# Optimization experiments

Hardware: AMD Instinct MI355X
Metric: run time of the kernel (lower is better)

Reference implementation:

```python
import jax, jax.numpy as jnp
import numpy as np

B, H_IMG, W_IMG = 8, 64, 64
C, HEADS, SR, MSG = 128, 4, 4, 4
N0 = H_IMG * W_IMG


def _linear(x, w, b):
    return x @ w.T + b


def _layernorm(x, g, b, eps=1e-5):
    mu = jnp.mean(x, -1, keepdims=True)
    var = jnp.mean(jnp.square(x - mu), -1, keepdims=True)
    return (x - mu) * jax.lax.rsqrt(var + eps) * g + b


def _conv2d(x, w, b, stride, pad, groups=1):
    y = jax.lax.conv_general_dilated(
        x, w, (stride, stride), [(pad, pad), (pad, pad)],
        dimension_numbers=("NCHW", "OIHW", "NCHW"), feature_group_count=groups)
    return y + b[None, :, None, None]


def setup_inputs():
    key = jax.random.key(0)
    ks = jax.random.split(key, 16)
    def nrm(k, shape, std=0.02):
        return jax.random.normal(k, shape, jnp.float32) * std
    z = lambda *s: jnp.zeros(s, jnp.float32)
    return {
        "x": jax.random.normal(ks[0], (B, N0, C), jnp.float32),
        "msg_tokens": jax.random.normal(ks[1], (B, MSG, C), jnp.float32),
        "Wq": nrm(ks[2], (C, C)), "bq": z(C),
        "sr1_w": nrm(ks[3], (C, C, 4, 4), float(np.sqrt(2.0 / (16 * C)))), "sr1_b": z(C),
        "ln1_g": jnp.ones((C,), jnp.float32), "ln1_b": z(C),
        "sr2_w": nrm(ks[4], (C, C, 2, 2), float(np.sqrt(2.0 / (4 * C)))), "sr2_b": z(C),
        "ln2_g": jnp.ones((C,), jnp.float32), "ln2_b": z(C),
        "kv1_w": nrm(ks[5], (C, C)), "kv1_b": z(C),
        "kv2_w": nrm(ks[6], (C, C)), "kv2_b": z(C),
        "lc1_w": nrm(ks[7], (C // 2, 1, 3, 3), float(np.sqrt(2.0 / 9.0))), "lc1_b": z(C // 2),
        "lc2_w": nrm(ks[8], (C // 2, 1, 3, 3), float(np.sqrt(2.0 / 9.0))), "lc2_b": z(C // 2),
        "proj_w": nrm(ks[9], (C, C)), "proj_b": z(C),
        "H": H_IMG, "W": W_IMG,
    }


def reference(x, msg_tokens, Wq, bq, sr1_w, sr1_b, ln1_g, ln1_b,
              sr2_w, sr2_b, ln2_g, ln2_b, kv1_w, kv1_b, kv2_w, kv2_b,
              lc1_w, lc1_b, lc2_w, lc2_b, proj_w, proj_b, H, W):
    Bsz, _, Cc = x.shape
    m = msg_tokens.shape[1]
    h = HEADS
    dh = Cc // h
    scale = dh ** -0.5
    x_q = jnp.concatenate([x, msg_tokens], axis=1)       # [B, N, C]
    N = x_q.shape[1]
    q = _linear(x_q, Wq, bq).reshape(Bsz, N, h, dh).transpose(0, 2, 1, 3)  # [B,h,N,dh]
    x_img = x.transpose(0, 2, 1).reshape(Bsz, Cc, H, W)

    def branch(sr_w, sr_b, ln_g, ln_b, kv_w, kv_b, lc_w, lc_b, q_half, stride):
        Hr, Wr = H // stride, W // stride
        L = Hr * Wr
        # spatial reduction conv -> tokens
        xr = _conv2d(x_img, sr_w, sr_b, stride, 0).reshape(Bsz, Cc, L).transpose(0, 2, 1)
        # message tokens pass through the SR conv via summed weights
        msg_r = jnp.einsum('bnc,oc->bno', msg_tokens, sr_w.sum((-1, -2))) + sr_b
        xk = jax.nn.gelu(_layernorm(jnp.concatenate([xr, msg_r], 1), ln_g, ln_b), approximate=False)
        kv = _linear(xk, kv_w, kv_b).reshape(Bsz, L + m, 2, h // 2, dh).transpose(2, 0, 3, 1, 4)
        k, v = kv[0], kv[1]                               # [B, h/2, L+m, dh]
        attn = jax.nn.softmax(jnp.einsum('bhnd,bhld->bhnl', q_half, k) * scale, axis=-1)
        # fused depthwise conv on the spatial part of V (message tokens bypass)
        v_flat = v.transpose(0, 2, 1, 3).reshape(Bsz, L + m, Cc // 2).transpose(0, 2, 1)  # [B,C/2,L+m]
        lc = _conv2d(v_flat[:, :, :L].reshape(Bsz, Cc // 2, Hr, Wr), lc_w, lc_b, 1, 1,
                     groups=Cc // 2).reshape(Bsz, Cc // 2, L)
        v_add = jnp.concatenate([lc, v_flat[:, :, L:]], axis=2)
        v = v + v_add.reshape(Bsz, h // 2, dh, L + m).transpose(0, 1, 3, 2)
        return jnp.einsum('bhnl,bhld->bhnd', attn, v).transpose(0, 2, 1, 3).reshape(Bsz, N, Cc // 2)

    x1 = branch(sr1_w, sr1_b, ln1_g, ln1_b, kv1_w, kv1_b, lc1_w, lc1_b, q[:, :h // 2], SR)
    x2 = branch(sr2_w, sr2_b, ln2_g, ln2_b, kv2_w, kv2_b, lc2_w, lc2_b, q[:, h // 2:], SR // 2)
    out = _linear(jnp.concatenate([x1, x2], -1), proj_w, proj_b)
    out = x_q + out                                       # identity = x_q, drop_path = Identity
    return out[:, :-m], out[:, -m:]
```

## Files before the change

### kernel.cpp

```cpp
#include <hip/hip_runtime.h>
#include <math.h>

#define BB 8
#define CC 128
#define N0 4096
#define MSGN 4
#define NTOT 4100
#define IMG 64
#define NPAD 4224
#define LMP1 320
#define LMP2 1088

#define OFF_WFQ    0
#define OFF_WFKV1  8192
#define OFF_WFKV2  16384
#define OFF_WFPROJ 24576
#define OFF_WFSR1  32768
#define OFF_WFSR2  163840
#define OFF_QH     196608
#define OFF_XK1    2359296
#define OFF_XK2    2492416
#define OFF_KV1O   3018752
#define OFF_KV2O   3284992
#define OFF_KH1    4337664
#define OFF_VT1    4419584
#define OFF_KH2    4501504
#define OFF_VT2    4780032
#define OFF_XP     5058560

typedef _Float16 half8v __attribute__((ext_vector_type(8)));
typedef _Float16 half4v __attribute__((ext_vector_type(4)));
typedef float f32x4 __attribute__((ext_vector_type(4)));

__device__ __forceinline__ size_t af_idx(int m, int k, int Kc) {
    return ((size_t)((m >> 4) * Kc + (k >> 5)) * 64 + ((k >> 3) & 3) * 16 + (m & 15)) * 8 + (k & 7);
}

__device__ __forceinline__ float exp2_fast(float x) {
#if __has_builtin(__builtin_amdgcn_exp2f)
    return __builtin_amdgcn_exp2f(x);
#else
    return __expf(x * 0.6931471805599453f);
#endif
}

__device__ __forceinline__ void gload16(const _Float16* g, _Float16* l) {
    __builtin_amdgcn_global_load_lds(
        (const __attribute__((address_space(1))) unsigned int*)g,
        (__attribute__((address_space(3))) unsigned int*)l, 16, 0, 0);
}

__global__ void prep_weights(const float* __restrict__ Wq, const float* __restrict__ kv1,
                             const float* __restrict__ kv2, const float* __restrict__ proj,
                             const float* __restrict__ sr1w, const float* __restrict__ sr2w,
                             float* __restrict__ ws, _Float16* __restrict__ Qh,
                             _Float16* __restrict__ Kh1, _Float16* __restrict__ Kh2) {
    int u = blockIdx.x * blockDim.x + threadIdx.x;
    if (u >= 176128) {
        int e = u - 176128;
        int d = e & 31;
        int rest = e >> 5;
        if (rest < 960) {
            int n = 260 + rest % 60;
            int bh = rest / 60;
            Kh1[((size_t)bh * LMP1 + n) * 32 + d] = (_Float16)0.f;
        } else {
            rest -= 960;
            int n = 1028 + rest % 60;
            int bh = rest / 60;
            Kh2[((size_t)bh * LMP2 + n) * 32 + d] = (_Float16)0.f;
        }
        return;
    }
    if (u >= 49152) {
        int idx = u - 49152;
        int d = idx & 31;
        int rest = idx >> 5;
        int n = NTOT + rest % (NPAD - NTOT);
        int rest2 = rest / (NPAD - NTOT);
        int hg = rest2 & 3;
        int b = rest2 >> 2;
        Qh[((size_t)(b * 4 + hg) * NPAD + n) * 32 + d] = (_Float16)0.f;
        return;
    }
    int seg, base;
    const float* w = nullptr;
    _Float16* dst;
    if (u < 2048)        { seg = 0; base = u;          w = Wq;   dst = (_Float16*)(ws + OFF_WFQ); }
    else if (u < 4096)   { seg = 0; base = u - 2048;   w = kv1;  dst = (_Float16*)(ws + OFF_WFKV1); }
    else if (u < 6144)   { seg = 0; base = u - 4096;   w = kv2;  dst = (_Float16*)(ws + OFF_WFKV2); }
    else if (u < 8192)   { seg = 0; base = u - 6144;   w = proj; dst = (_Float16*)(ws + OFF_WFPROJ); }
    else if (u < 40960)  { seg = 1; base = u - 8192;   w = sr1w; dst = (_Float16*)(ws + OFF_WFSR1); }
    else                 { seg = 2; base = u - 40960;  w = sr2w; dst = (_Float16*)(ws + OFF_WFSR2); }
    int lane = base & 63;
    int t = (base >> 6) & 7;
    int kc = base >> 9;
    int n = t * 16 + (lane & 15);
    int k0 = kc * 32 + (lane >> 4) * 8;
    half8v val;
    #pragma unroll
    for (int j = 0; j < 8; ++j) {
        int k = k0 + j;
        float v;
        if (seg == 0) v = w[n * 128 + k];
        else if (seg == 1) v = w[(n * 128 + (k & 127)) * 16 + (k >> 7)];
        else v = w[(n * 128 + (k & 127)) * 4 + (k >> 7)];
        val[j] = (_Float16)v;
    }
    *(half8v*)(dst + (size_t)base * 8) = val;
}

template<int S, int WR, int LL, int LM, int KW>
__device__ __forceinline__ void sr_partial(
    int mtile, int kcbase, int lane, const float* __restrict__ x,
    const float* __restrict__ msg, const _Float16* __restrict__ Wf, f32x4 acc[8]) {
    int m15 = lane & 15, quadk = lane >> 4;
    int m = mtile * 16 + m15;
    bool valid = m < BB * LM;
    const float* base = x;
    bool isimg = false;
    if (valid) {
        int b = m / LM, tok = m - b * LM;
        if (tok < LL) {
            int hr = tok / WR, wr = tok - hr * WR;
            base = x + ((size_t)b * N0 + hr * S * IMG + wr * S) * 128;
            isimg = true;
        } else {
            base = msg + ((size_t)b * MSGN + (tok - LL)) * 128;
        }
    }
    const half8v* Bp = (const half8v*)Wf + lane;
    for (int kk = 0; kk < KW; ++kk) {
        int kc = kcbase + kk;
        int k0 = (kc * 4 + quadk) * 8;
        int c = k0 & 127, ij = k0 >> 7;
        half8v a;
        if (valid) {
            int off;
            if (isimg) {
                int ki = ij / S, kj = ij - ki * S;
                off = (ki * IMG + kj) * 128 + c;
            } else off = c;
            const float4* p4 = (const float4*)(base + off);
            float4 f0 = p4[0], f1 = p4[1];
            a[0] = (_Float16)f0.x; a[1] = (_Float16)f0.y; a[2] = (_Float16)f0.z; a[3] = (_Float16)f0.w;
            a[4] = (_Float16)f1.x; a[5] = (_Float16)f1.y; a[6] = (_Float16)f1.z; a[7] = (_Float16)f1.w;
        } else {
            #pragma unroll
            for (int j = 0; j < 8; ++j) a[j] = (_Float16)0.f;
        }
        #pragma unroll
        for (int t = 0; t < 8; ++t)
            acc[t] = __builtin_amdgcn_mfma_f32_16x16x32_f16(a, Bp[(size_t)(kc * 8 + t) * 64], acc[t], 0, 0, 0);
    }
}

__global__ __launch_bounds__(256) void input_gemms(
    const float* __restrict__ x, const float* __restrict__ msg,
    const _Float16* __restrict__ Wf1, const _Float16* __restrict__ Wf2,
    const float* __restrict__ b1, const float* __restrict__ g1, const float* __restrict__ be1,
    const float* __restrict__ b2, const float* __restrict__ g2, const float* __restrict__ be2,
    const _Float16* __restrict__ WfKV1, const _Float16* __restrict__ WfKV2,
    const float* __restrict__ kvb1, const float* __restrict__ kvb2,
    _Float16* __restrict__ Kh1, float* __restrict__ vo1,
    _Float16* __restrict__ Kh2, float* __restrict__ vo2,
    const _Float16* __restrict__ WfQ, const float* __restrict__ bq,
    _Float16* __restrict__ Qh) {
    __shared__ float red[4][2048];
    int tid = threadIdx.x;
    int lane = tid & 63, wave = tid >> 6;
    int bid = blockIdx.x;
    const f32x4 zf4 = {0.f, 0.f, 0.f, 0.f};

    if (bid >= 261) {
        int u = (bid - 261) * 4 + wave;
        int mt = u >> 1, nh = u & 1;
        int m15 = lane & 15, quadk = lane >> 4;
        int m = mt * 16 + m15;
        bool valid = m < BB * NTOT;
        const float* rowp = x;
        if (valid) {
            int b = m / NTOT, n = m - b * NTOT;
            rowp = (n < N0) ? (x + ((size_t)b * N0 + n) * 128)
                            : (msg + ((size_t)b * MSGN + (n - N0)) * 128);
        }
        const half8v* Bp = (const half8v*)WfQ + lane;
        f32x4 acc[4];
        #pragma unroll
        for (int t = 0; t < 4; ++t) acc[t] = zf4;
        #pragma unroll
        for (int kc = 0; kc < 4; ++kc) {
            half8v a;
            if (valid) {
                const float4* p4 = (const float4*)(rowp + (kc * 4 + quadk) * 8);
                float4 f0 = p4[0], f1 = p4[1];
                a[0] = (_Float16)f0.x; a[1] = (_Float16)f0.y; a[2] = (_Float16)f0.z; a[3] = (_Float16)f0.w;
                a[4] = (_Float16)f1.x; a[5] = (_Float16)f1.y; a[6] = (_Float16)f1.z; a[7] = (_Float16)f1.w;
            } else {
                #pragma unroll
                for (int j = 0; j < 8; ++j) a[j] = (_Float16)0.f;
            }
            #pragma unroll
            for (int t = 0; t < 4; ++t)
                acc[t] = __builtin_amdgcn_mfma_f32_16x16x32_f16(a, Bp[(size_t)(kc * 8 + nh * 4 + t) * 64], acc[t], 0, 0, 0);
        }
        int quad = lane >> 4, n15 = lane & 15;
        const float qscale = 0.17677669529663687f * 1.4426950408889634f;
        #pragma unroll
        for (int r = 0; r < 4; ++r) {
            int mm = mt * 16 + quad * 4 + r;
            if (mm >= BB * NTOT) continue;
            int b = mm / NTOT, tok = mm - b * NTOT;
            #pragma unroll
            for (int t = 0; t < 4; ++t) {
                int n = nh * 64 + t * 16 + n15;
                Qh[((size_t)(b * 4 + (n >> 5)) * NPAD + tok) * 32 + (n & 31)] =
                    (_Float16)((acc[t][r] + bq[n]) * qscale);
            }
        }
        return;
    }

    if (bid >= 132) {
        int mtile = (bid - 132) * 4 + wave;
        f32x4 acc[8];
        #pragma unroll
        for (int t = 0; t < 8; ++t) acc[t] = zf4;
        sr_partial<2, 32, 1024, 1028, 16>(mtile, 0, lane, x, msg, Wf2, acc);
        int quad = lane >> 4, n15 = lane & 15;
        float bb[8], gg[8], eb[8];
        #pragma unroll
        for (int j = 0; j < 8; ++j) {
            bb[j] = b2[j * 16 + n15];
            gg[j] = g2[j * 16 + n15];
            eb[j] = be2[j * 16 + n15];
        }
        _Float16* XKw = (_Float16*)(&red[0][0]) + wave * 2176;
        #pragma unroll
        for (int r = 0; r < 4; ++r) {
            float s = 0.f;
            #pragma unroll
            for (int j = 0; j < 8; ++j) s += acc[j][r] + bb[j];
            #pragma unroll
            for (int off = 1; off < 16; off <<= 1) s += __shfl_xor(s, off);
            float mu = s * (1.f / 128.f);
            float q = 0.f;
            #pragma unroll
            for (int j = 0; j < 8; ++j) { float d = acc[j][r] + bb[j] - mu; q += d * d; }
            #pragma unroll
            for (int off = 1; off < 16; off <<= 1) q += __shfl_xor(q, off);
            float rs = rsqrtf(q * (1.f / 128.f) + 1e-5f);
            #pragma unroll
            for (int j = 0; j < 8; ++j) {
                float y = (acc[j][r] + bb[j] - mu) * rs * gg[j] + eb[j];
                y = 0.5f * y * (1.f + erff(y * 0.70710678118654752f));
                XKw[(quad * 4 + r) * 136 + j * 16 + n15] = (_Float16)y;
            }
        }
        __syncthreads();
        const half8v* Bp = (const half8v*)WfKV2 + lane;
        f32x4 ka[8];
        #pragma unroll
        for (int tt = 0; tt < 8; ++tt) ka[tt] = zf4;
        #pragma unroll
        for (int kc = 0; kc < 4; ++kc) {
            half8v a = *(const half8v*)&XKw[(lane & 15) * 136 + kc * 32 + (lane >> 4) * 8];
            #pragma unroll
            for (int tt = 0; tt < 8; ++tt)
                ka[tt] = __builtin_amdgcn_mfma_f32_16x16x32_f16(a, Bp[(size_t)(kc * 8 + tt) * 64], ka[tt], 0, 0, 0);
        }
        #pragma unroll
        for (int r = 0; r < 4; ++r) {
            int m = mtile * 16 + quad * 4 + r;
            if (m >= 8224) continue;
            int b = m / 1028, tok = m - b * 1028;
            #pragma unroll
            for (int tt = 0; tt < 8; ++tt) {
                int n = tt * 16 + n15;
                float val = ka[tt][r] + kvb2[n];
                if (tt < 4) {
                    Kh2[((size_t)(b * 2 + (n >> 5)) * LMP2 + tok) * 32 + (n & 31)] = (_Float16)val;
                } else {
                    vo2[((size_t)b * 1028 + tok) * 64 + (n - 64)] = val;
                }
            }
        }
        return;
    }

    f32x4 acc[8];
    #pragma unroll
    for (int t = 0; t < 8; ++t) acc[t] = zf4;
    int mtile = bid;
    sr_partial<4, 16, 256, 260, 16>(mtile, wave * 16, lane, x, msg, Wf1, acc);
    int quad = lane >> 4, n15 = lane & 15;
    #pragma unroll
    for (int t = 0; t < 8; ++t)
        #pragma unroll
        for (int r = 0; r < 4; ++r)
            red[wave][(quad * 4 + r) * 128 + t * 16 + n15] = acc[t][r];
    __syncthreads();
    for (int e = tid; e < 2048; e += 256)
        red[0][e] = red[0][e] + red[1][e] + red[2][e] + red[3][e];
    __syncthreads();
    int r16 = tid >> 4, l16 = tid & 15;
    int m = mtile * 16 + r16;
    float v[8];
    float s = 0.f;
    #pragma unroll
    for (int j = 0; j < 8; ++j) { v[j] = red[0][r16 * 128 + j * 16 + l16] + b1[j * 16 + l16]; s += v[j]; }
    #pragma unroll
    for (int off = 1; off < 16; off <<= 1) s += __shfl_xor(s, off);
    float mu = s * (1.f / 128.f);
    float q = 0.f;
    #pragma unroll
    for (int j = 0; j < 8; ++j) { v[j] -= mu; q += v[j] * v[j]; }
    #pragma unroll
    for (int off = 1; off < 16; off <<= 1) q += __shfl_xor(q, off);
    float rs = rsqrtf(q * (1.f / 128.f) + 1e-5f);
    _Float16* XKs = (_Float16*)(&red[1][0]);
    if (m < 2080) {
        #pragma unroll
        for (int j = 0; j < 8; ++j) {
            float y = v[j] * rs * g1[j * 16 + l16] + be1[j * 16 + l16];
            y = 0.5f * y * (1.f + erff(y * 0.70710678118654752f));
            XKs[r16 * 136 + j * 16 + l16] = (_Float16)y;
        }
    }
    __syncthreads();
    {
        const half8v* Bp = (const half8v*)WfKV1 + lane;
        int t0 = wave * 2;
        f32x4 ka[2];
        ka[0] = zf4; ka[1] = zf4;
        #pragma unroll
        for (int kc = 0; kc < 4; ++kc) {
            half8v a = *(const half8v*)&XKs[(lane & 15) * 136 + kc * 32 + (lane >> 4) * 8];
            #pragma unroll
            for (int tt = 0; tt < 2; ++tt)
                ka[tt] = __builtin_amdgcn_mfma_f32_16x16x32_f16(a, Bp[(size_t)(kc * 8 + t0 + tt) * 64], ka[tt], 0, 0, 0);
        }
        #pragma unroll
        for (int r = 0; r < 4; ++r) {
            int mm = mtile * 16 + quad * 4 + r;
            if (mm >= 2080) continue;
            int b = mm / 260, tok = mm - b * 260;
            #pragma unroll
            for (int tt = 0; tt < 2; ++tt) {
                int n = (t0 + tt) * 16 + n15;
                float val = ka[tt][r] + kvb1[n];
                if (n < 64) {
                    Kh1[((size_t)(b * 2 + (n >> 5)) * LMP1 + tok) * 32 + (n & 31)] = (_Float16)val;
                } else {
                    vo1[((size_t)b * 260 + tok) * 64 + (n - 64)] = val;
                }
            }
        }
    }
}

__global__ void pack_kv(const float* __restrict__ vo1, const float* __restrict__ vo2,
                        const float* __restrict__ lc1w, const float* __restrict__ lc1b,
                        const float* __restrict__ lc2w, const float* __restrict__ lc2b,
                        _Float16* __restrict__ Vt1, _Float16* __restrict__ Vt2) {
    int idx = blockIdx.x * 256 + threadIdx.x;
    const int T1 = BB * LMP1 * 64;
    const float* vo;
    const float* lcw;
    const float* lcb;
    _Float16* Vt;
    int Wr, L, Lm, Lmp, li;
    if (idx < T1) { li = idx;      vo = vo1; lcw = lc1w; lcb = lc1b; Vt = Vt1; Wr = 16; L = 256;  Lm = 260;  Lmp = LMP1; }
    else          { li = idx - T1; vo = vo2; lcw = lc2w; lcb = lc2b; Vt = Vt2; Wr = 32; L = 1024; Lm = 1028; Lmp = LMP2; }
    int ch = li & 63;
    int rest = li >> 6;
    int n = rest % Lmp;
    int b = rest / Lmp;
    int h2 = ch >> 5, d = ch & 31;
    int Hr = L / Wr;
    float vnew = 0.f;
    if (n < Lm) {
        const float* vb2 = vo + (size_t)b * Lm * 64;
        float v = vb2[(size_t)n * 64 + ch];
        float add;
        if (n < L) {
            int hr = n / Wr, wr = n - hr * Wr;
            float sum = lcb[ch];
            #pragma unroll
            for (int ki = 0; ki < 3; ++ki)
                #pragma unroll
                for (int kj = 0; kj < 3; ++kj) {
                    int y = hr + ki - 1, xx = wr + kj - 1;
                    if ((unsigned)y < (unsigned)Hr && (unsigned)xx < (unsigned)Wr)
                        sum += lcw[ch * 9 + ki * 3 + kj] * vb2[((size_t)y * Wr + xx) * 64 + ch];
                }
            add = sum;
        } else {
            add = v;
        }
        vnew = v + add;
    }
    Vt[(size_t)(b * 2 + h2) * Lmp * 32 + (size_t)(n >> 2) * 128
       + (d & 15) * 8 + ((d >> 4) << 2) + (n & 3)] = (_Float16)vnew;
}

__global__ __launch_bounds__(256, 4) void attn_mfma(
    const _Float16* __restrict__ Qh,
    const _Float16* __restrict__ Kh1, const _Float16* __restrict__ Vt1,
    const _Float16* __restrict__ Kh2, const _Float16* __restrict__ Vt2,
    _Float16* __restrict__ XP) {
    __shared__ _Float16 sK[3][2048];
    __shared__ _Float16 sV[3][2048];
    int tid = threadIdx.x;
    int lane = tid & 63, wave = tid >> 6;
    int b = blockIdx.y;
    int z = blockIdx.z;
    int h2 = z & 1, br = 1 - (z >> 1);
    int tile = blockIdx.x * 4 + wave;
    int n0 = tile * 32;
    int q16 = lane & 15, quad = lane >> 4;
    const f32x4 zf = {0.f, 0.f, 0.f, 0.f};
    int NT = br ? (LMP2 / 64) : (LMP1 / 64);
    int Lmp = br ? LMP2 : LMP1;
    const _Float16* kb = (br ? Kh2 : Kh1) + (size_t)(b * 2 + h2) * Lmp * 32;
    const _Float16* vb = (br ? Vt2 : Vt1) + (size_t)(b * 2 + h2) * Lmp * 32;
    int hg = br * 2 + h2;
    const _Float16* qp = Qh + ((size_t)(b * 4 + hg) * NPAD + n0 + q16) * 32 + quad * 8;
    half8v qf0 = *(const half8v*)qp;
    half8v qf1 = *(const half8v*)(qp + 512);
    f32x4 O00 = zf, O01 = zf, O10 = zf, O11 = zf;
    f32x4 La = zf, Lb = zf;
    half4v ones4;
    #pragma unroll
    for (int r = 0; r < 4; ++r) ones4[r] = (_Float16)1.f;

    int ksrc = (wave * 16 + q16) * 32 + quad * 8;
    int vsrc = wave * 512 + lane * 8;

    gload16(kb + ksrc, &sK[0][wave * 512]);
    gload16(vb + vsrc, &sV[0][wave * 512]);
    gload16(kb + 2048 + ksrc, &sK[1][wave * 512]);
    gload16(vb + 2048 + vsrc, &sV[1][wave * 512]);
    asm volatile("s_waitcnt vmcnt(2)" ::: "memory");
    __builtin_amdgcn_sched_barrier(0);
    __builtin_amdgcn_s_barrier();

    for (int t = 0; t < NT; ++t) {
        int cur = t % 3;
        if (t + 2 < NT) {
            int nxt = (t + 2) % 3;
            size_t o = (size_t)(t + 2) * 2048;
            gload16(kb + o + ksrc, &sK[nxt][wave * 512]);
            gload16(vb + o + vsrc, &sV[nxt][wave * 512]);
        }
        half8v kf[4], vv[4];
        #pragma unroll
        for (int i = 0; i < 4; ++i)
            kf[i] = *(const half8v*)&sK[cur][i * 512 + lane * 8];
        #pragma unroll
        for (int i = 0; i < 4; ++i)
            vv[i] = *(const half8v*)&sV[cur][i * 512 + quad * 128 + q16 * 8];

        __builtin_amdgcn_s_setprio(1);
        half4v p0[4], p1[4];
        #pragma unroll
        for (int i = 0; i < 4; ++i) {
            f32x4 s0 = __builtin_amdgcn_mfma_f32_16x16x32_f16(kf[i], qf0, zf, 0, 0, 0);
            f32x4 s1 = __builtin_amdgcn_mfma_f32_16x16x32_f16(kf[i], qf1, zf, 0, 0, 0);
            half4v a, c;
            #pragma unroll
            for (int r = 0; r < 4; ++r) {
                a[r] = (_Float16)exp2_fast(s0[r]);
                c[r] = (_Float16)exp2_fast(s1[r]);
            }
            p0[i] = a; p1[i] = c;
        }
        #pragma unroll
        for (int i = 0; i < 4; ++i) {
            half4v v0 = __builtin_shufflevector(vv[i], vv[i], 0, 1, 2, 3);
            half4v v1 = __builtin_shufflevector(vv[i], vv[i], 4, 5, 6, 7);
            O00 = __builtin_amdgcn_mfma_f32_16x16x16f16(p0[i], v0, O00, 0, 0, 0);
            O01 = __builtin_amdgcn_mfma_f32_16x16x16f16(p0[i], v1, O01, 0, 0, 0);
            La  = __builtin_amdgcn_mfma_f32_16x16x16f16(p0[i], ones4, La, 0, 0, 0);
            O10 = __builtin_amdgcn_mfma_f32_16x16x16f16(p1[i], v0, O10, 0, 0, 0);
            O11 = __builtin_amdgcn_mfma_f32_16x16x16f16(p1[i], v1, O11, 0, 0, 0);
            Lb  = __builtin_amdgcn_mfma_f32_16x16x16f16(p1[i], ones4, Lb, 0, 0, 0);
        }
        __builtin_amdgcn_s_setprio(0);

        if (t + 2 < NT) asm volatile("s_waitcnt vmcnt(2)" ::: "memory");
        else            asm volatile("s_waitcnt vmcnt(0)" ::: "memory");
        __builtin_amdgcn_sched_barrier(0);
        __builtin_amdgcn_s_barrier();
    }

    int kbase = br * 64 + h2 * 32;
    #pragma unroll
    for (int r = 0; r < 4; ++r) {
        float fa = 1.0f / (La[r] - 60.0f);
        float fb = 1.0f / (Lb[r] - 60.0f);
        int n = n0 + quad * 4 + r;
        if (n < NTOT) {
            int m = b * NTOT + n;
            XP[af_idx(m, kbase + q16, 4)] = (_Float16)(O00[r] * fa);
            XP[af_idx(m, kbase + 16 + q16, 4)] = (_Float16)(O01[r] * fa);
        }
        int n2 = n + 16;
        if (n2 < NTOT) {
            int m = b * NTOT + n2;
            XP[af_idx(m, kbase + q16, 4)] = (_Float16)(O10[r] * fb);
            XP[af_idx(m, kbase + 16 + q16, 4)] = (_Float16)(O11[r] * fb);
        }
    }
}

__global__ __launch_bounds__(256) void proj_gemm(
    const _Float16* __restrict__ XP,
    const _Float16* __restrict__ Wf, const float* __restrict__ bias,
    float* __restrict__ out_f32, const float* __restrict__ x, const float* __restrict__ msg) {
    int lane = threadIdx.x & 63, wave = threadIdx.x >> 6;
    int u = blockIdx.x * 4 + wave;
    int mt = u >> 1, nh = u & 1;
    const half8v* Ap = (const half8v*)XP + (size_t)mt * 4 * 64 + lane;
    const half8v* Bp = (const half8v*)Wf + lane;
    f32x4 acc[4];
    #pragma unroll
    for (int t = 0; t < 4; ++t) acc[t] = (f32x4){0.f, 0.f, 0.f, 0.f};
    #pragma unroll
    for (int kc = 0; kc < 4; ++kc) {
        half8v a = Ap[(size_t)kc * 64];
        #pragma unroll
        for (int t = 0; t < 4; ++t)
            acc[t] = __builtin_amdgcn_mfma_f32_16x16x32_f16(a, Bp[(size_t)(kc * 8 + nh * 4 + t) * 64], acc[t], 0, 0, 0);
    }
    int quad = lane >> 4, n15 = lane & 15;
    #pragma unroll
    for (int r = 0; r < 4; ++r) {
        int m = mt * 16 + quad * 4 + r;
        if (m >= BB * NTOT) continue;
        int b = m / NTOT, tok = m - b * NTOT;
        const float* rp;
        float* dst;
        if (tok < N0) {
            rp = x + ((size_t)b * N0 + tok) * 128;
            dst = out_f32 + ((size_t)b * N0 + tok) * 128;
        } else {
            rp = msg + ((size_t)b * MSGN + (tok - N0)) * 128;
            dst = out_f32 + (size_t)BB * N0 * 128 + ((size_t)b * MSGN + (tok - N0)) * 128;
        }
        #pragma unroll
        for (int t = 0; t < 4; ++t) {
            int n = nh * 64 + t * 16 + n15;
            dst[n] = acc[t][r] + bias[n] + rp[n];
        }
    }
}

extern "C" void kernel_launch(void* const* d_in, const int* in_sizes, int n_in,
                              void* d_out, int out_size, void* d_ws, size_t ws_size,
                              hipStream_t stream) {
    const float* x     = (const float*)d_in[0];
    const float* msg   = (const float*)d_in[1];
    const float* Wq    = (const float*)d_in[2];
    const float* bq    = (const float*)d_in[3];
    const float* sr1w  = (const float*)d_in[4];
    const float* sr1b  = (const float*)d_in[5];
    const float* ln1g  = (const float*)d_in[6];
    const float* ln1b  = (const float*)d_in[7];
    const float* sr2w  = (const float*)d_in[8];
    const float* sr2b  = (const float*)d_in[9];
    const float* ln2g  = (const float*)d_in[10];
    const float* ln2b  = (const float*)d_in[11];
    const float* kv1w  = (const float*)d_in[12];
    const float* kv1b  = (const float*)d_in[13];
    const float* kv2w  = (const float*)d_in[14];
    const float* kv2b  = (const float*)d_in[15];
    const float* lc1w  = (const float*)d_in[16];
    const float* lc1b  = (const float*)d_in[17];
    const float* lc2w  = (const float*)d_in[18];
    const float* lc2b  = (const float*)d_in[19];
    const float* projw = (const float*)d_in[20];
    const float* projb = (const float*)d_in[21];
    float* ws  = (float*)d_ws;
    float* out = (float*)d_out;

    _Float16* WfQ    = (_Float16*)(ws + OFF_WFQ);
    _Float16* WfKV1  = (_Float16*)(ws + OFF_WFKV1);
    _Float16* WfKV2  = (_Float16*)(ws + OFF_WFKV2);
    _Float16* WfPROJ = (_Float16*)(ws + OFF_WFPROJ);
    _Float16* WfSR1  = (_Float16*)(ws + OFF_WFSR1);
    _Float16* WfSR2  = (_Float16*)(ws + OFF_WFSR2);
    _Float16* Qh     = (_Float16*)(ws + OFF_QH);
    _Float16* XP     = (_Float16*)(ws + OFF_XP);
    float* vo1       = ws + OFF_KV1O;
    float* vo2       = ws + OFF_KV2O;
    _Float16* Kh1    = (_Float16*)(ws + OFF_KH1);
    _Float16* Vt1    = (_Float16*)(ws + OFF_VT1);
    _Float16* Kh2    = (_Float16*)(ws + OFF_KH2);
    _Float16* Vt2    = (_Float16*)(ws + OFF_VT2);

    prep_weights<<<928, 256, 0, stream>>>(Wq, kv1w, kv2w, projw, sr1w, sr2w, ws, Qh, Kh1, Kh2);
    input_gemms<<<1286, 256, 0, stream>>>(x, msg, WfSR1, WfSR2,
                                          sr1b, ln1g, ln1b, sr2b, ln2g, ln2b,
                                          WfKV1, WfKV2, kv1b, kv2b,
                                          Kh1, vo1, Kh2, vo2,
                                          WfQ, bq, Qh);
    pack_kv<<<2816, 256, 0, stream>>>(vo1, vo2, lc1w, lc1b, lc2w, lc2b, Vt1, Vt2);
    attn_mfma<<<dim3(33, 8, 4), 256, 0, stream>>>(Qh, Kh1, Vt1, Kh2, Vt2, XP);
    proj_gemm<<<1025, 256, 0, stream>>>(XP, WfPROJ, projb, out, x, msg);
}
```

Baseline: 186.0 us.

## Widen attention blocks to eight waves sharing K/V tiles, template pack_kv

The attention kernel now runs 512-thread blocks of eight query waves, so each K/V tile staged into LDS serves twice as many query tiles. The split K and V buffers become one combined triple-buffered array, and each thread issues a single async load per stage. NPAD and the prep_weights grid are enlarged to pad Q for the coarser tiling. pack_kv is templated per branch so shapes become compile-time constants. The larger blocks cut the grid roughly in half, which may reduce occupancy and wave-level parallelism.

```diff
diff --git a/kernel.cpp b/kernel.cpp
--- a/kernel.cpp
+++ b/kernel.cpp
@@ -7,7 +7,7 @@
 #define MSGN 4
 #define NTOT 4100
 #define IMG 64
-#define NPAD 4224
+#define NPAD 4352
 #define LMP1 320
 #define LMP2 1088
 
@@ -18,8 +18,6 @@
 #define OFF_WFSR1  32768
 #define OFF_WFSR2  163840
 #define OFF_QH     196608
-#define OFF_XK1    2359296
-#define OFF_XK2    2492416
 #define OFF_KV1O   3018752
 #define OFF_KV2O   3284992
 #define OFF_KH1    4337664
@@ -56,8 +54,8 @@
                              float* __restrict__ ws, _Float16* __restrict__ Qh,
                              _Float16* __restrict__ Kh1, _Float16* __restrict__ Kh2) {
     int u = blockIdx.x * blockDim.x + threadIdx.x;
-    if (u >= 176128) {
-        int e = u - 176128;
+    if (u >= 307200) {
+        int e = u - 307200;
         int d = e & 31;
         int rest = e >> 5;
         if (rest < 960) {
@@ -359,25 +357,17 @@
     }
 }
 
-__global__ void pack_kv(const float* __restrict__ vo1, const float* __restrict__ vo2,
-                        const float* __restrict__ lc1w, const float* __restrict__ lc1b,
-                        const float* __restrict__ lc2w, const float* __restrict__ lc2b,
-                        _Float16* __restrict__ Vt1, _Float16* __restrict__ Vt2) {
-    int idx = blockIdx.x * 256 + threadIdx.x;
-    const int T1 = BB * LMP1 * 64;
-    const float* vo;
-    const float* lcw;
-    const float* lcb;
-    _Float16* Vt;
-    int Wr, L, Lm, Lmp, li;
-    if (idx < T1) { li = idx;      vo = vo1; lcw = lc1w; lcb = lc1b; Vt = Vt1; Wr = 16; L = 256;  Lm = 260;  Lmp = LMP1; }
-    else          { li = idx - T1; vo = vo2; lcw = lc2w; lcb = lc2b; Vt = Vt2; Wr = 32; L = 1024; Lm = 1028; Lmp = LMP2; }
+template<int Wr, int L, int Lm, int Lmp>
+__device__ __forceinline__ void pack_one(int li, const float* __restrict__ vo,
+                                         const float* __restrict__ lcw,
+                                         const float* __restrict__ lcb,
+                                         _Float16* __restrict__ Vt) {
     int ch = li & 63;
     int rest = li >> 6;
     int n = rest % Lmp;
     int b = rest / Lmp;
     int h2 = ch >> 5, d = ch & 31;
-    int Hr = L / Wr;
+    const int Hr = L / Wr;
     float vnew = 0.f;
     if (n < Lm) {
         const float* vb2 = vo + (size_t)b * Lm * 64;
@@ -404,19 +394,28 @@
        + (d & 15) * 8 + ((d >> 4) << 2) + (n & 3)] = (_Float16)vnew;
 }
 
-__global__ __launch_bounds__(256, 4) void attn_mfma(
+__global__ void pack_kv(const float* __restrict__ vo1, const float* __restrict__ vo2,
+                        const float* __restrict__ lc1w, const float* __restrict__ lc1b,
+                        const float* __restrict__ lc2w, const float* __restrict__ lc2b,
+                        _Float16* __restrict__ Vt1, _Float16* __restrict__ Vt2) {
+    int idx = blockIdx.x * 256 + threadIdx.x;
+    const int T1 = BB * LMP1 * 64;
+    if (idx < T1) pack_one<16, 256, 260, LMP1>(idx, vo1, lc1w, lc1b, Vt1);
+    else          pack_one<32, 1024, 1028, LMP2>(idx - T1, vo2, lc2w, lc2b, Vt2);
+}
+
+__global__ __launch_bounds__(512, 4) void attn_mfma(
     const _Float16* __restrict__ Qh,
     const _Float16* __restrict__ Kh1, const _Float16* __restrict__ Vt1,
     const _Float16* __restrict__ Kh2, const _Float16* __restrict__ Vt2,
     _Float16* __restrict__ XP) {
-    __shared__ _Float16 sK[3][2048];
-    __shared__ _Float16 sV[3][2048];
+    __shared__ _Float16 sT[3][4096];
     int tid = threadIdx.x;
     int lane = tid & 63, wave = tid >> 6;
     int b = blockIdx.y;
     int z = blockIdx.z;
     int h2 = z & 1, br = 1 - (z >> 1);
-    int tile = blockIdx.x * 4 + wave;
+    int tile = blockIdx.x * 8 + wave;
     int n0 = tile * 32;
     int q16 = lane & 15, quad = lane >> 4;
     const f32x4 zf = {0.f, 0.f, 0.f, 0.f};
@@ -434,14 +433,16 @@
     #pragma unroll
     for (int r = 0; r < 4; ++r) ones4[r] = (_Float16)1.f;
 
-    int ksrc = (wave * 16 + q16) * 32 + quad * 8;
-    int vsrc = wave * 512 + lane * 8;
-
-    gload16(kb + ksrc, &sK[0][wave * 512]);
-    gload16(vb + vsrc, &sV[0][wave * 512]);
-    gload16(kb + 2048 + ksrc, &sK[1][wave * 512]);
-    gload16(vb + 2048 + vsrc, &sV[1][wave * 512]);
-    asm volatile("s_waitcnt vmcnt(2)" ::: "memory");
+    int isK = tid < 256;
+    int st = isK ? tid : tid - 256;
+    int ssub = st >> 6, sl = st & 63;
+    int ksrc = (ssub * 16 + (sl & 15)) * 32 + (sl >> 4) * 8;
+    const _Float16* gsrc = isK ? (kb + ksrc) : (vb + st * 8);
+    int doff = isK ? (st * 8) : (2048 + st * 8);
+
+    gload16(gsrc, &sT[0][doff]);
+    gload16(gsrc + 2048, &sT[1][doff]);
+    asm volatile("s_waitcnt vmcnt(1)" ::: "memory");
     __builtin_amdgcn_sched_barrier(0);
     __builtin_amdgcn_s_barrier();
 
@@ -449,17 +450,15 @@
         int cur = t % 3;
         if (t + 2 < NT) {
             int nxt = (t + 2) % 3;
-            size_t o = (size_t)(t + 2) * 2048;
-            gload16(kb + o + ksrc, &sK[nxt][wave * 512]);
-            gload16(vb + o + vsrc, &sV[nxt][wave * 512]);
+            gload16(gsrc + (size_t)(t + 2) * 2048, &sT[nxt][doff]);
         }
         half8v kf[4], vv[4];
         #pragma unroll
         for (int i = 0; i < 4; ++i)
-            kf[i] = *(const half8v*)&sK[cur][i * 512 + lane * 8];
+            kf[i] = *(const half8v*)&sT[cur][i * 512 + lane * 8];
         #pragma unroll
         for (int i = 0; i < 4; ++i)
-            vv[i] = *(const half8v*)&sV[cur][i * 512 + quad * 128 + q16 * 8];
+            vv[i] = *(const half8v*)&sT[cur][2048 + i * 512 + quad * 128 + q16 * 8];
 
         __builtin_amdgcn_s_setprio(1);
         half4v p0[4], p1[4];
@@ -488,7 +487,7 @@
         }
         __builtin_amdgcn_s_setprio(0);
 
-        if (t + 2 < NT) asm volatile("s_waitcnt vmcnt(2)" ::: "memory");
+        if (t + 2 < NT) asm volatile("s_waitcnt vmcnt(1)" ::: "memory");
         else            asm volatile("s_waitcnt vmcnt(0)" ::: "memory");
         __builtin_amdgcn_sched_barrier(0);
         __builtin_amdgcn_s_barrier();
@@ -599,13 +598,13 @@
     _Float16* Kh2    = (_Float16*)(ws + OFF_KH2);
     _Float16* Vt2    = (_Float16*)(ws + OFF_VT2);
 
-    prep_weights<<<928, 256, 0, stream>>>(Wq, kv1w, kv2w, projw, sr1w, sr2w, ws, Qh, Kh1, Kh2);
+    prep_weights<<<1440, 256, 0, stream>>>(Wq, kv1w, kv2w, projw, sr1w, sr2w, ws, Qh, Kh1, Kh2);
     input_gemms<<<1286, 256, 0, stream>>>(x, msg, WfSR1, WfSR2,
                                           sr1b, ln1g, ln1b, sr2b, ln2g, ln2b,
                                           WfKV1, WfKV2, kv1b, kv2b,
                                           Kh1, vo1, Kh2, vo2,
                                           WfQ, bq, Qh);
     pack_kv<<<2816, 256, 0, stream>>>(vo1, vo2, lc1w, lc1b, lc2w, lc2b, Vt1, Vt2);
-    attn_mfma<<<dim3(33, 8, 4), 256, 0, stream>>>(Qh, Kh1, Vt1, Kh2, Vt2, XP);
+    attn_mfma<<<dim3(17, 8, 4), 512, 0, stream>>>(Qh, Kh1, Vt1, Kh2, Vt2, XP);
     proj_gemm<<<1025, 256, 0, stream>>>(XP, WfPROJ, projb, out, x, msg);
 }
```

Result: slower. 190.3 us (+2.3%).

## Fuse Q projection into attention kernel, drop Qh buffer and padding writes

Applied to the files above, without the earlier changes.

Moves the Q linear projection from input_gemms into the attention kernel. Each wave computes its own 32-row Q tile with MFMA from x/msg, stages it through LDS, and then loads the Q fragments from there. This removes the Qh global round trip, the Q padding zero-fill in prep_weights, and about a thousand blocks from input_gemms. In exchange the attention kernel reads fp32 x rows and recomputes the projection in each kernel instance, and it adds LDS use and prologue latency. pack_kv is also templated so its constants specialise at compile time.

```diff
diff --git a/kernel.cpp b/kernel.cpp
--- a/kernel.cpp
+++ b/kernel.cpp
@@ -7,7 +7,6 @@
 #define MSGN 4
 #define NTOT 4100
 #define IMG 64
-#define NPAD 4224
 #define LMP1 320
 #define LMP2 1088
 
@@ -17,9 +16,6 @@
 #define OFF_WFPROJ 24576
 #define OFF_WFSR1  32768
 #define OFF_WFSR2  163840
-#define OFF_QH     196608
-#define OFF_XK1    2359296
-#define OFF_XK2    2492416
 #define OFF_KV1O   3018752
 #define OFF_KV2O   3284992
 #define OFF_KH1    4337664
@@ -53,11 +49,11 @@
 __global__ void prep_weights(const float* __restrict__ Wq, const float* __restrict__ kv1,
                              const float* __restrict__ kv2, const float* __restrict__ proj,
                              const float* __restrict__ sr1w, const float* __restrict__ sr2w,
-                             float* __restrict__ ws, _Float16* __restrict__ Qh,
+                             float* __restrict__ ws,
                              _Float16* __restrict__ Kh1, _Float16* __restrict__ Kh2) {
     int u = blockIdx.x * blockDim.x + threadIdx.x;
-    if (u >= 176128) {
-        int e = u - 176128;
+    if (u >= 49152) {
+        int e = u - 49152;
         int d = e & 31;
         int rest = e >> 5;
         if (rest < 960) {
@@ -70,17 +66,6 @@
             int bh = rest / 60;
             Kh2[((size_t)bh * LMP2 + n) * 32 + d] = (_Float16)0.f;
         }
-        return;
-    }
-    if (u >= 49152) {
-        int idx = u - 49152;
-        int d = idx & 31;
-        int rest = idx >> 5;
-        int n = NTOT + rest % (NPAD - NTOT);
-        int rest2 = rest / (NPAD - NTOT);
-        int hg = rest2 & 3;
-        int b = rest2 >> 2;
-        Qh[((size_t)(b * 4 + hg) * NPAD + n) * 32 + d] = (_Float16)0.f;
         return;
     }
     int seg, base;
@@ -163,63 +148,12 @@
     const _Float16* __restrict__ WfKV1, const _Float16* __restrict__ WfKV2,
     const float* __restrict__ kvb1, const float* __restrict__ kvb2,
     _Float16* __restrict__ Kh1, float* __restrict__ vo1,
-    _Float16* __restrict__ Kh2, float* __restrict__ vo2,
-    const _Float16* __restrict__ WfQ, const float* __restrict__ bq,
-    _Float16* __restrict__ Qh) {
+    _Float16* __restrict__ Kh2, float* __restrict__ vo2) {
     __shared__ float red[4][2048];
     int tid = threadIdx.x;
     int lane = tid & 63, wave = tid >> 6;
     int bid = blockIdx.x;
     const f32x4 zf4 = {0.f, 0.f, 0.f, 0.f};
-
-    if (bid >= 261) {
-        int u = (bid - 261) * 4 + wave;
-        int mt = u >> 1, nh = u & 1;
-        int m15 = lane & 15, quadk = lane >> 4;
-        int m = mt * 16 + m15;
-        bool valid = m < BB * NTOT;
-        const float* rowp = x;
-        if (valid) {
-            int b = m / NTOT, n = m - b * NTOT;
-            rowp = (n < N0) ? (x + ((size_t)b * N0 + n) * 128)
-                            : (msg + ((size_t)b * MSGN + (n - N0)) * 128);
-        }
-        const half8v* Bp = (const half8v*)WfQ + lane;
-        f32x4 acc[4];
-        #pragma unroll
-        for (int t = 0; t < 4; ++t) acc[t] = zf4;
-        #pragma unroll
-        for (int kc = 0; kc < 4; ++kc) {
-            half8v a;
-            if (valid) {
-                const float4* p4 = (const float4*)(rowp + (kc * 4 + quadk) * 8);
-                float4 f0 = p4[0], f1 = p4[1];
-                a[0] = (_Float16)f0.x; a[1] = (_Float16)f0.y; a[2] = (_Float16)f0.z; a[3] = (_Float16)f0.w;
-                a[4] = (_Float16)f1.x; a[5] = (_Float16)f1.y; a[6] = (_Float16)f1.z; a[7] = (_Float16)f1.w;
-            } else {
-                #pragma unroll
-                for (int j = 0; j < 8; ++j) a[j] = (_Float16)0.f;
-            }
-            #pragma unroll
-            for (int t = 0; t < 4; ++t)
-                acc[t] = __builtin_amdgcn_mfma_f32_16x16x32_f16(a, Bp[(size_t)(kc * 8 + nh * 4 + t) * 64], acc[t], 0, 0, 0);
-        }
-        int quad = lane >> 4, n15 = lane & 15;
-        const float qscale = 0.17677669529663687f * 1.4426950408889634f;
-        #pragma unroll
-        for (int r = 0; r < 4; ++r) {
-            int mm = mt * 16 + quad * 4 + r;
-            if (mm >= BB * NTOT) continue;
-            int b = mm / NTOT, tok = mm - b * NTOT;
-            #pragma unroll
-            for (int t = 0; t < 4; ++t) {
-                int n = nh * 64 + t * 16 + n15;
-                Qh[((size_t)(b * 4 + (n >> 5)) * NPAD + tok) * 32 + (n & 31)] =
-                    (_Float16)((acc[t][r] + bq[n]) * qscale);
-            }
-        }
-        return;
-    }
 
     if (bid >= 132) {
         int mtile = (bid - 132) * 4 + wave;
@@ -359,25 +293,17 @@
     }
 }
 
-__global__ void pack_kv(const float* __restrict__ vo1, const float* __restrict__ vo2,
-                        const float* __restrict__ lc1w, const float* __restrict__ lc1b,
-                        const float* __restrict__ lc2w, const float* __restrict__ lc2b,
-                        _Float16* __restrict__ Vt1, _Float16* __restrict__ Vt2) {
-    int idx = blockIdx.x * 256 + threadIdx.x;
-    const int T1 = BB * LMP1 * 64;
-    const float* vo;
-    const float* lcw;
-    const float* lcb;
-    _Float16* Vt;
-    int Wr, L, Lm, Lmp, li;
-    if (idx < T1) { li = idx;      vo = vo1; lcw = lc1w; lcb = lc1b; Vt = Vt1; Wr = 16; L = 256;  Lm = 260;  Lmp = LMP1; }
-    else          { li = idx - T1; vo = vo2; lcw = lc2w; lcb = lc2b; Vt = Vt2; Wr = 32; L = 1024; Lm = 1028; Lmp = LMP2; }
+template<int Wr, int L, int Lm, int Lmp>
+__device__ __forceinline__ void pack_one(int li, const float* __restrict__ vo,
+                                         const float* __restrict__ lcw,
+                                         const float* __restrict__ lcb,
+                                         _Float16* __restrict__ Vt) {
     int ch = li & 63;
     int rest = li >> 6;
     int n = rest % Lmp;
     int b = rest / Lmp;
     int h2 = ch >> 5, d = ch & 31;
-    int Hr = L / Wr;
+    const int Hr = L / Wr;
     float vnew = 0.f;
     if (n < Lm) {
         const float* vb2 = vo + (size_t)b * Lm * 64;
@@ -404,13 +330,25 @@
        + (d & 15) * 8 + ((d >> 4) << 2) + (n & 3)] = (_Float16)vnew;
 }
 
+__global__ void pack_kv(const float* __restrict__ vo1, const float* __restrict__ vo2,
+                        const float* __restrict__ lc1w, const float* __restrict__ lc1b,
+                        const float* __restrict__ lc2w, const float* __restrict__ lc2b,
+                        _Float16* __restrict__ Vt1, _Float16* __restrict__ Vt2) {
+    int idx = blockIdx.x * 256 + threadIdx.x;
+    const int T1 = BB * LMP1 * 64;
+    if (idx < T1) pack_one<16, 256, 260, LMP1>(idx, vo1, lc1w, lc1b, Vt1);
+    else          pack_one<32, 1024, 1028, LMP2>(idx - T1, vo2, lc2w, lc2b, Vt2);
+}
+
 __global__ __launch_bounds__(256, 4) void attn_mfma(
-    const _Float16* __restrict__ Qh,
+    const float* __restrict__ x, const float* __restrict__ msg,
+    const _Float16* __restrict__ WfQ, const float* __restrict__ bq,
     const _Float16* __restrict__ Kh1, const _Float16* __restrict__ Vt1,
     const _Float16* __restrict__ Kh2, const _Float16* __restrict__ Vt2,
     _Float16* __restrict__ XP) {
     __shared__ _Float16 sK[3][2048];
     __shared__ _Float16 sV[3][2048];
+    __shared__ _Float16 sQ[4][1024];
     int tid = threadIdx.x;
     int lane = tid & 63, wave = tid >> 6;
     int b = blockIdx.y;
@@ -425,14 +363,6 @@
     const _Float16* kb = (br ? Kh2 : Kh1) + (size_t)(b * 2 + h2) * Lmp * 32;
     const _Float16* vb = (br ? Vt2 : Vt1) + (size_t)(b * 2 + h2) * Lmp * 32;
     int hg = br * 2 + h2;
-    const _Float16* qp = Qh + ((size_t)(b * 4 + hg) * NPAD + n0 + q16) * 32 + quad * 8;
-    half8v qf0 = *(const half8v*)qp;
-    half8v qf1 = *(const half8v*)(qp + 512);
-    f32x4 O00 = zf, O01 = zf, O10 = zf, O11 = zf;
-    f32x4 La = zf, Lb = zf;
-    half4v ones4;
-    #pragma unroll
-    for (int r = 0; r < 4; ++r) ones4[r] = (_Float16)1.f;
 
     int ksrc = (wave * 16 + q16) * 32 + quad * 8;
     int vsrc = wave * 512 + lane * 8;
@@ -441,7 +371,54 @@
     gload16(vb + vsrc, &sV[0][wave * 512]);
     gload16(kb + 2048 + ksrc, &sK[1][wave * 512]);
     gload16(vb + 2048 + vsrc, &sV[1][wave * 512]);
-    asm volatile("s_waitcnt vmcnt(2)" ::: "memory");
+
+    {
+        _Float16* qlds = &sQ[wave][0];
+        const half8v* BpQ = (const half8v*)WfQ + lane;
+        const float qscale = 0.17677669529663687f * 1.4426950408889634f;
+        #pragma unroll
+        for (int s = 0; s < 2; ++s) {
+            int row = n0 + s * 16 + q16;
+            bool valid = row < NTOT;
+            const float* rowp = x;
+            if (valid)
+                rowp = (row < N0) ? (x + ((size_t)b * N0 + row) * 128)
+                                  : (msg + ((size_t)b * MSGN + (row - N0)) * 128);
+            f32x4 qa0 = zf, qa1 = zf;
+            #pragma unroll
+            for (int kc = 0; kc < 4; ++kc) {
+                half8v a;
+                if (valid) {
+                    const float4* p4 = (const float4*)(rowp + (kc * 4 + quad) * 8);
+                    float4 f0 = p4[0], f1 = p4[1];
+                    a[0] = (_Float16)f0.x; a[1] = (_Float16)f0.y; a[2] = (_Float16)f0.z; a[3] = (_Float16)f0.w;
+                    a[4] = (_Float16)f1.x; a[5] = (_Float16)f1.y; a[6] = (_Float16)f1.z; a[7] = (_Float16)f1.w;
+                } else {
+                    #pragma unroll
+                    for (int j = 0; j < 8; ++j) a[j] = (_Float16)0.f;
+                }
+                qa0 = __builtin_amdgcn_mfma_f32_16x16x32_f16(a, BpQ[(size_t)(kc * 8 + hg * 2) * 64], qa0, 0, 0, 0);
+                qa1 = __builtin_amdgcn_mfma_f32_16x16x32_f16(a, BpQ[(size_t)(kc * 8 + hg * 2 + 1) * 64], qa1, 0, 0, 0);
+            }
+            #pragma unroll
+            for (int r = 0; r < 4; ++r) {
+                int rl = s * 16 + quad * 4 + r;
+                qlds[rl * 32 + q16]      = (_Float16)((qa0[r] + bq[hg * 32 + q16]) * qscale);
+                qlds[rl * 32 + 16 + q16] = (_Float16)((qa1[r] + bq[hg * 32 + 16 + q16]) * qscale);
+            }
+        }
+    }
+    _Float16* qlds = &sQ[wave][0];
+    half8v qf0 = *(const half8v*)&qlds[q16 * 32 + quad * 8];
+    half8v qf1 = *(const half8v*)&qlds[(16 + q16) * 32 + quad * 8];
+
+    f32x4 O00 = zf, O01 = zf, O10 = zf, O11 = zf;
+    f32x4 La = zf, Lb = zf;
+    half4v ones4;
+    #pragma unroll
+    for (int r = 0; r < 4; ++r) ones4[r] = (_Float16)1.f;
+
+    asm volatile("s_waitcnt vmcnt(1)" ::: "memory");
     __builtin_amdgcn_sched_barrier(0);
     __builtin_amdgcn_s_barrier();
 
@@ -590,7 +567,6 @@
     _Float16* WfPROJ = (_Float16*)(ws + OFF_WFPROJ);
     _Float16* WfSR1  = (_Float16*)(ws + OFF_WFSR1);
     _Float16* WfSR2  = (_Float16*)(ws + OFF_WFSR2);
-    _Float16* Qh     = (_Float16*)(ws + OFF_QH);
     _Float16* XP     = (_Float16*)(ws + OFF_XP);
     float* vo1       = ws + OFF_KV1O;
     float* vo2       = ws + OFF_KV2O;
@@ -599,13 +575,13 @@
     _Float16* Kh2    = (_Float16*)(ws + OFF_KH2);
     _Float16* Vt2    = (_Float16*)(ws + OFF_VT2);
 
-    prep_weights<<<928, 256, 0, stream>>>(Wq, kv1w, kv2w, projw, sr1w, sr2w, ws, Qh, Kh1, Kh2);
-    input_gemms<<<1286, 256, 0, stream>>>(x, msg, WfSR1, WfSR2,
-                                          sr1b, ln1g, ln1b, sr2b, ln2g, ln2b,
-                                          WfKV1, WfKV2, kv1b, kv2b,
-                                          Kh1, vo1, Kh2, vo2,
-                                          WfQ, bq, Qh);
+    prep_weights<<<432, 256, 0, stream>>>(Wq, kv1w, kv2w, projw, sr1w, sr2w, ws, Kh1, Kh2);
+    input_gemms<<<261, 256, 0, stream>>>(x, msg, WfSR1, WfSR2,
+                                         sr1b, ln1g, ln1b, sr2b, ln2g, ln2b,
+                                         WfKV1, WfKV2, kv1b, kv2b,
+                                         Kh1, vo1, Kh2, vo2);
     pack_kv<<<2816, 256, 0, stream>>>(vo1, vo2, lc1w, lc1b, lc2w, lc2b, Vt1, Vt2);
-    attn_mfma<<<dim3(33, 8, 4), 256, 0, stream>>>(Qh, Kh1, Vt1, Kh2, Vt2, XP);
+    attn_mfma<<<dim3(33, 8, 4), 256, 0, stream>>>(x, msg, WfQ, bq,
+                                                  Kh1, Vt1, Kh2, Vt2, XP);
     proj_gemm<<<1025, 256, 0, stream>>>(XP, WfPROJ, projb, out, x, msg);
 }
```

Measured after the change: 190.7 us. 2.5% more time.
